# Optimization experiments

Measured on AMD Instinct MI355X. Metric: run time of the kernel, lower is better.

## Reference

```python
import jax, jax.numpy as jnp
import numpy as np
from functools import partial

S, E, K = 50000, 20000, 128
B = 16384
NE = 1000000
L = 2  # num_layer


def setup_inputs() -> dict:
    key = jax.random.key(0)
    ks = jax.random.split(key, 24)
    inp = {
        'stu_id': jax.random.randint(ks[0], (B,), 0, S),
        'input_exercise': jax.random.randint(ks[1], (B,), 0, E),
        'input_knowledge_point': jax.random.uniform(ks[2], (B, K), jnp.float32),
        'rows_1': jax.random.randint(ks[3], (NE,), 0, S),
        'cols_1': jax.random.randint(ks[4], (NE,), 0, E),
        'rows_0': jax.random.randint(ks[5], (NE,), 0, S),
        'cols_0': jax.random.randint(ks[6], (NE,), 0, E),
        'vals_ui_1': jax.random.uniform(ks[7], (NE,), jnp.float32),
        'vals_iu_1': jax.random.uniform(ks[8], (NE,), jnp.float32),
        'vals_ui_0': jax.random.uniform(ks[9], (NE,), jnp.float32),
        'vals_iu_0': jax.random.uniform(ks[10], (NE,), jnp.float32),
        'd_i_1': jax.random.uniform(ks[11], (S,), jnp.float32),
        'd_j_1': jax.random.uniform(ks[12], (E,), jnp.float32),
        'd_i_0': jax.random.uniform(ks[13], (S,), jnp.float32),
        'd_j_0': jax.random.uniform(ks[14], (E,), jnp.float32),
        'student_emb': jax.random.normal(ks[15], (S, K), jnp.float32) * 0.1,
        'exercise_emb': jax.random.normal(ks[16], (E, K), jnp.float32) * 0.1,
        'student_emb_bias': jax.random.normal(ks[17], (S, 1), jnp.float32) * 0.1,
        'e_discrimination': jax.random.normal(ks[18], (E, 1), jnp.float32) * 0.1,
        'W1': jax.random.normal(ks[19], (256, K), jnp.float32) * (1.0 / np.sqrt(K)),
        'b1': jnp.zeros((256,), jnp.float32),
        'W2': jax.random.normal(ks[20], (128, 256), jnp.float32) * (1.0 / np.sqrt(256)),
        'b2': jnp.zeros((128,), jnp.float32),
        'W3': jax.random.normal(ks[21], (1, 128), jnp.float32) * (1.0 / np.sqrt(128)),
        'b3': jnp.zeros((1,), jnp.float32),
    }
    return inp


def pos_linear(x, W, b):
    # PosLinear: weight = 2*relu(-W) + W  (== |W|)
    Wp = 2.0 * jax.nn.relu(-W) + W
    return x @ Wp.T + b


def spmm(vals, rows, cols, x, n_out):
    # sparse.mm(A, x) where A has entries vals at (rows, cols); gather cols of x, scatter-add to rows
    return jax.ops.segment_sum(vals[:, None] * x[cols], rows, num_segments=n_out)


def graph_repr(student_emb, exercise_emb,
               rows_1, cols_1, vals_ui_1, vals_iu_1,
               rows_0, cols_0, vals_ui_0, vals_iu_0,
               d_i_1, d_j_1, d_i_0, d_j_0):
    stat = student_emb          # [S, K]
    kdiff = exercise_emb        # [E, K]
    for _ in range(L):
        u1 = spmm(vals_ui_1, rows_1, cols_1, kdiff, S) + stat * d_i_1[:, None]
        i1 = spmm(vals_iu_1, cols_1, rows_1, stat, E) + kdiff * d_j_1[:, None]
        u0 = spmm(vals_ui_0, rows_0, cols_0, kdiff, S) + stat * d_i_0[:, None]
        i0 = spmm(vals_iu_0, cols_0, rows_0, stat, E) + kdiff * d_j_0[:, None]
        stat = u1 + u0
        kdiff = i1 + i0
    return stat, kdiff


def reference(stu_id, input_exercise, input_knowledge_point,
              rows_1, cols_1, rows_0, cols_0,
              vals_ui_1, vals_iu_1, vals_ui_0, vals_iu_0,
              d_i_1, d_j_1, d_i_0, d_j_0,
              student_emb, exercise_emb, student_emb_bias, e_discrimination,
              W1, b1, W2, b2, W3, b3):
    stat, kdiff = graph_repr(student_emb, exercise_emb,
                             rows_1, cols_1, vals_ui_1, vals_iu_1,
                             rows_0, cols_0, vals_ui_0, vals_iu_0,
                             d_i_1, d_j_1, d_i_0, d_j_0)
    e_disc = jax.nn.sigmoid(e_discrimination[input_exercise])          # [B, 1]
    stat_b = jax.nn.sigmoid(stat[stu_id] + student_emb_bias[stu_id])   # [B, K]
    kd = jax.nn.sigmoid(kdiff[input_exercise])                         # [B, K]
    x = input_knowledge_point * (stat_b - kd) * e_disc
    x = jnp.tanh(pos_linear(x, W1, b1))   # dropout is identity in eval
    x = jnp.tanh(pos_linear(x, W2, b2))
    out = jax.nn.sigmoid(pos_linear(x, W3, b3))
    return out.reshape(-1)
```

## Files before the change

### kernel.cpp

```cpp
#include <hip/hip_runtime.h>
#include <hip/hip_fp16.h>

#define S_N 50000
#define E_N 20000
#define K_N 128
#define B_N 16384
#define NE_N 1000000

#define S_PER_XCD 6250
#define E_PER_XCD 2500

#define SCAP 96
#define ECAP 176

#define NBKT 512
#define S_SUB 196
#define E_SUB 79
#define BKCAP 8704
#define OVL_BKTS 257

typedef short bf16x8 __attribute__((ext_vector_type(8)));
typedef float f32x4 __attribute__((ext_vector_type(4)));
typedef int i32x4 __attribute__((ext_vector_type(4)));
typedef float f32x4v __attribute__((ext_vector_type(4)));

__device__ __forceinline__ float sigmoidf_(float v) {
    return 1.0f / (1.0f + __expf(-v));
}
__device__ __forceinline__ float tanh_fast(float v) {
    float e = __expf(2.0f * v);
    return 1.0f - 2.0f / (e + 1.0f);
}
__device__ __forceinline__ unsigned short f2bf(float v) {
    unsigned u = __float_as_uint(v);
    u += 0x7fffu + ((u >> 16) & 1u);
    return (unsigned short)(u >> 16);
}
__device__ __forceinline__ void split_bf(float v, unsigned short& hi, unsigned short& lo) {
    unsigned u = __float_as_uint(v);
    hi = (unsigned short)(u >> 16);
    float fh = __uint_as_float(u & 0xffff0000u);
    lo = f2bf(v - fh);
}
__device__ __forceinline__ void accum8(float* acc, uint4 h, float v) {
    float2 p0 = __half22float2(*(const __half2*)&h.x);
    float2 p1 = __half22float2(*(const __half2*)&h.y);
    float2 p2 = __half22float2(*(const __half2*)&h.z);
    float2 p3 = __half22float2(*(const __half2*)&h.w);
    acc[0] = fmaf(v, p0.x, acc[0]); acc[1] = fmaf(v, p0.y, acc[1]);
    acc[2] = fmaf(v, p1.x, acc[2]); acc[3] = fmaf(v, p1.y, acc[3]);
    acc[4] = fmaf(v, p2.x, acc[4]); acc[5] = fmaf(v, p2.y, acc[5]);
    acc[6] = fmaf(v, p3.x, acc[6]); acc[7] = fmaf(v, p3.y, acc[7]);
}

__device__ __forceinline__ unsigned long long* bslot(
    unsigned long long* ovl, unsigned long long* fr, int b) {
    return (b < OVL_BKTS) ? ovl + (size_t)b * BKCAP
                          : fr + (size_t)(b - OVL_BKTS) * BKCAP;
}

__global__ __launch_bounds__(1024) void bucketize2(
    const i32x4* __restrict__ r1, const i32x4* __restrict__ c1,
    const f32x4v* __restrict__ vui1, const f32x4v* __restrict__ viu1,
    const i32x4* __restrict__ r0, const i32x4* __restrict__ c0,
    const f32x4v* __restrict__ vui0, const f32x4v* __restrict__ viu0,
    unsigned long long* __restrict__ bOvl, unsigned long long* __restrict__ bFr,
    int* __restrict__ gcur) {
    __shared__ int hist[NBKT];
    __shared__ int base[NBKT];
    const int tid = threadIdx.x;
    for (int b = tid; b < NBKT; b += 1024) hist[b] = 0;
    __syncthreads();
    const int NV = NE_N / 4;
    i32x4 rv[2], cv[2]; f32x4v av[2], bv[2];
    int bkt[16], lr[16];
#pragma unroll
    for (int rep = 0; rep < 2; ++rep) {
        int i = blockIdx.x * 2048 + rep * 1024 + tid;
        bool valid = i < 2 * NV;
        if (valid) {
            if (i < NV) {
                rv[rep] = __builtin_nontemporal_load(r1 + i);
                cv[rep] = __builtin_nontemporal_load(c1 + i);
                av[rep] = __builtin_nontemporal_load(vui1 + i);
                bv[rep] = __builtin_nontemporal_load(viu1 + i);
            } else {
                int j = i - NV;
                rv[rep] = __builtin_nontemporal_load(r0 + j);
                cv[rep] = __builtin_nontemporal_load(c0 + j);
                av[rep] = __builtin_nontemporal_load(vui0 + j);
                bv[rep] = __builtin_nontemporal_load(viu0 + j);
            }
        }
#pragma unroll
        for (int k = 0; k < 4; ++k) {
            int u = rep * 8 + k * 2;
            if (valid) {
                int r = rv[rep][k], c = cv[rep][k];
                int xs = r / S_PER_XCD;
                int ss = (r - xs * S_PER_XCD) / S_SUB;
                int xe = c / E_PER_XCD;
                int se = (c - xe * E_PER_XCD) / E_SUB;
                bkt[u] = ss * 8 + xs;
                bkt[u + 1] = 256 + se * 8 + xe;
                lr[u] = atomicAdd(&hist[bkt[u]], 1);
                lr[u + 1] = atomicAdd(&hist[bkt[u + 1]], 1);
            } else {
                bkt[u] = -1; bkt[u + 1] = -1;
            }
        }
    }
    __syncthreads();
    for (int b = tid; b < NBKT; b += 1024) {
        int h = hist[b];
        base[b] = h ? atomicAdd(&gcur[b], h) : 0;
    }
    __syncthreads();
#pragma unroll
    for (int rep = 0; rep < 2; ++rep) {
#pragma unroll
        for (int k = 0; k < 4; ++k) {
            int u = rep * 8 + k * 2;
            if (bkt[u] >= 0) {
                int r = rv[rep][k], c = cv[rep][k];
                unsigned entS = ((unsigned)f2bf(av[rep][k]) << 16) | (unsigned)c;
                unsigned entE = ((unsigned)f2bf(bv[rep][k]) << 16) | (unsigned)r;
                int pS = base[bkt[u]] + lr[u];
                int pE = base[bkt[u + 1]] + lr[u + 1];
                if (pS < BKCAP)
                    bslot(bOvl, bFr, bkt[u])[pS] =
                        ((unsigned long long)(unsigned)r << 32) | entS;
                if (pE < BKCAP)
                    bslot(bOvl, bFr, bkt[u + 1])[pE] =
                        ((unsigned long long)(unsigned)c << 32) | entE;
            }
        }
    }
}

__global__ __launch_bounds__(256) void scatter2(
    unsigned long long* __restrict__ bOvl, unsigned long long* __restrict__ bFr,
    const int* __restrict__ gcur,
    int* __restrict__ cntS, int* __restrict__ cntE,
    unsigned* __restrict__ csrS, unsigned* __restrict__ csrE) {
    __shared__ int lcnt[S_SUB];
    const int bid = blockIdx.x;
    const int tid = threadIdx.x;
    const bool isS = bid < 256;
    const int x = bid & 7;
    const int s = (isS ? bid : bid - 256) >> 3;
    const int start = isS ? x * S_PER_XCD + s * S_SUB : x * E_PER_XCD + s * E_SUB;
    const int len = isS ? min(S_SUB, S_PER_XCD - s * S_SUB)
                        : min(E_SUB, E_PER_XCD - s * E_SUB);
    for (int l = tid; l < len; l += 256) lcnt[l] = 0;
    __syncthreads();
    int n = gcur[bid];
    if (n > BKCAP) n = BKCAP;
    const unsigned long long* bp = bslot(bOvl, bFr, bid);
    for (int i = tid; i < n; i += 256) {
        unsigned long long v = __builtin_nontemporal_load(bp + i);
        int node = (int)(v >> 32);
        unsigned entry = (unsigned)v;
        int slot = atomicAdd(&lcnt[node - start], 1);
        if (isS) {
            if (slot < SCAP) csrS[(size_t)node * SCAP + slot] = entry;
        } else {
            if (slot < ECAP) csrE[(size_t)node * ECAP + slot] = entry;
        }
    }
    __syncthreads();
    for (int l = tid; l < len; l += 256) {
        if (isS) cntS[start + l] = lcnt[l];
        else     cntE[start + l] = lcnt[l];
    }
}

__global__ __launch_bounds__(256) void mark_needed2(
    const int* __restrict__ sid, const int* __restrict__ eid,
    unsigned* __restrict__ maskS, unsigned* __restrict__ maskE) {
    int i = blockIdx.x * blockDim.x + threadIdx.x;
    if (i < B_N) {
        int v = sid[i];
        atomicOr(&maskS[v >> 5], 1u << (v & 31));
    } else if (i < 2 * B_N) {
        int v = eid[i - B_N];
        atomicOr(&maskE[v >> 5], 1u << (v & 31));
    }
}

__global__ __launch_bounds__(256) void cvt_f16_init(
    const float2* __restrict__ sE, const float2* __restrict__ eE,
    __half2* __restrict__ sH, __half2* __restrict__ eH,
    int* __restrict__ cntS, int* __restrict__ cntE,
    unsigned* __restrict__ maskS, unsigned* __restrict__ maskE,
    int* __restrict__ cur) {
    int i = blockIdx.x * 256 + threadIdx.x;
    if (i < S_N) cntS[i] = 0;
    if (i < E_N) cntE[i] = 0;
    if (i < 2048) maskS[i] = 0;
    if (i < 1024) maskE[i] = 0;
    if (i < NBKT) cur[i] = 0;
    const int nS = S_N * 64;
    if (i < nS) {
        float2 v = sE[i];
        sH[i] = __floats2half2_rn(v.x, v.y);
    } else {
        int j = i - nS;
        if (j < E_N * 64) {
            float2 v = eE[j];
            eH[j] = __floats2half2_rn(v.x, v.y);
        }
    }
}

template<int CAP>
__global__ __launch_bounds__(256) void gather_pass_h4(
    const uint4* __restrict__ src, const uint4* __restrict__ self,
    const float* __restrict__ dA, const float* __restrict__ dB,
    const int* __restrict__ cnt, const unsigned* __restrict__ csr,
    const unsigned* __restrict__ need,
    uint4* __restrict__ dst, int nrow) {
    int w = blockIdx.x * 4 + (threadIdx.x >> 6);
    int lane = threadIdx.x & 63;
    int slot = lane >> 4;
    int seg = lane & 15;
    if (w >= nrow) return;
    if (need && !((need[w >> 5] >> (w & 31)) & 1u)) return;
    int n = cnt[w];
    if (n > CAP) n = CAP;
    const unsigned* cbase = csr + (size_t)w * CAP;
    float acc[8] = {};
    int i = 0;
    for (; i + 16 <= n; i += 16) {
        unsigned qa = __builtin_nontemporal_load(cbase + i + slot);
        unsigned qb = __builtin_nontemporal_load(cbase + i + 4 + slot);
        unsigned qc = __builtin_nontemporal_load(cbase + i + 8 + slot);
        unsigned qd = __builtin_nontemporal_load(cbase + i + 12 + slot);
        uint4 ha = src[(size_t)(qa & 0xffffu) * 16 + seg];
        uint4 hb = src[(size_t)(qb & 0xffffu) * 16 + seg];
        uint4 hc = src[(size_t)(qc & 0xffffu) * 16 + seg];
        uint4 hd = src[(size_t)(qd & 0xffffu) * 16 + seg];
        accum8(acc, ha, __uint_as_float(qa & 0xffff0000u));
        accum8(acc, hb, __uint_as_float(qb & 0xffff0000u));
        accum8(acc, hc, __uint_as_float(qc & 0xffff0000u));
        accum8(acc, hd, __uint_as_float(qd & 0xffff0000u));
    }
    for (; i + 8 <= n; i += 8) {
        unsigned qa = __builtin_nontemporal_load(cbase + i + slot);
        unsigned qb = __builtin_nontemporal_load(cbase + i + 4 + slot);
        uint4 ha = src[(size_t)(qa & 0xffffu) * 16 + seg];
        uint4 hb = src[(size_t)(qb & 0xffffu) * 16 + seg];
        accum8(acc, ha, __uint_as_float(qa & 0xffff0000u));
        accum8(acc, hb, __uint_as_float(qb & 0xffff0000u));
    }
    for (; i < n; i += 4) {
        int e = i + slot;
        if (e < n) {
            unsigned q = __builtin_nontemporal_load(cbase + e);
            uint4 h = src[(size_t)(q & 0xffffu) * 16 + seg];
            accum8(acc, h, __uint_as_float(q & 0xffff0000u));
        }
    }
#pragma unroll
    for (int j = 0; j < 8; ++j) {
        acc[j] += __shfl_xor(acc[j], 16);
        acc[j] += __shfl_xor(acc[j], 32);
    }
    if (slot == 0) {
        uint4 hs = self[(size_t)w * 16 + seg];
        float d = dA[w] + dB[w];
        float2 s0 = __half22float2(*(const __half2*)&hs.x);
        float2 s1 = __half22float2(*(const __half2*)&hs.y);
        float2 s2 = __half22float2(*(const __half2*)&hs.z);
        float2 s3 = __half22float2(*(const __half2*)&hs.w);
        uint4 o;
        *(__half2*)&o.x = __floats2half2_rn(fmaf(s0.x, d, acc[0]), fmaf(s0.y, d, acc[1]));
        *(__half2*)&o.y = __floats2half2_rn(fmaf(s1.x, d, acc[2]), fmaf(s1.y, d, acc[3]));
        *(__half2*)&o.z = __floats2half2_rn(fmaf(s2.x, d, acc[4]), fmaf(s2.y, d, acc[5]));
        *(__half2*)&o.w = __floats2half2_rn(fmaf(s3.x, d, acc[6]), fmaf(s3.y, d, acc[7]));
        dst[(size_t)w * 16 + seg] = o;
    }
}

__global__ __launch_bounds__(256) void abs_split_kernel(
    const float* __restrict__ W1, const float* __restrict__ W2,
    unsigned short* __restrict__ w1hi, unsigned short* __restrict__ w1lo,
    unsigned short* __restrict__ w2hi, unsigned short* __restrict__ w2lo) {
    int i = blockIdx.x * 256 + threadIdx.x;
    unsigned short hi, lo;
    if (i < 32768) {
        split_bf(fabsf(W1[i]), hi, lo);
        w1hi[i] = hi; w1lo[i] = lo;
    } else {
        int j = i - 32768;
        split_bf(fabsf(W2[j]), hi, lo);
        w2hi[j] = hi; w2lo[j] = lo;
    }
}

__global__ __launch_bounds__(256) void feature_kernel(
    const int* __restrict__ stu_id, const int* __restrict__ ex_id,
    const float* __restrict__ ikp,
    const __half2* __restrict__ statH, const __half2* __restrict__ kdiffH,
    const float* __restrict__ s_bias, const float* __restrict__ e_disc,
    unsigned short* __restrict__ xhi, unsigned short* __restrict__ xlo) {
    int i = blockIdx.x * 256 + threadIdx.x;
    int row = i >> 5;
    int k4 = (i & 31) * 4;
    int s = stu_id[row];
    int e = ex_id[row];
    float sb = s_bias[s];
    float ed = sigmoidf_(e_disc[e]);
    float2 s01 = __half22float2(statH[(size_t)s * 64 + (k4 >> 1)]);
    float2 s23 = __half22float2(statH[(size_t)s * 64 + (k4 >> 1) + 1]);
    float2 k01 = __half22float2(kdiffH[(size_t)e * 64 + (k4 >> 1)]);
    float2 k23 = __half22float2(kdiffH[(size_t)e * 64 + (k4 >> 1) + 1]);
    float4 iv = *(const float4*)(ikp + (size_t)row * K_N + k4);
    float f0 = iv.x * (sigmoidf_(s01.x + sb) - sigmoidf_(k01.x)) * ed;
    float f1 = iv.y * (sigmoidf_(s01.y + sb) - sigmoidf_(k01.y)) * ed;
    float f2 = iv.z * (sigmoidf_(s23.x + sb) - sigmoidf_(k23.x)) * ed;
    float f3 = iv.w * (sigmoidf_(s23.y + sb) - sigmoidf_(k23.y)) * ed;
    ushort4 oh, ol;
    split_bf(f0, oh.x, ol.x);
    split_bf(f1, oh.y, ol.y);
    split_bf(f2, oh.z, ol.z);
    split_bf(f3, oh.w, ol.w);
    *(ushort4*)(xhi + (size_t)row * K_N + k4) = oh;
    *(ushort4*)(xlo + (size_t)row * K_N + k4) = ol;
}

#define H1S 264

__global__ __launch_bounds__(256) void mlp_mfma(
    const unsigned short* __restrict__ xhi, const unsigned short* __restrict__ xlo,
    const unsigned short* __restrict__ w1hi, const unsigned short* __restrict__ w1lo,
    const unsigned short* __restrict__ w2hi, const unsigned short* __restrict__ w2lo,
    const float* __restrict__ b1, const float* __restrict__ b2,
    const float* __restrict__ W3, const float* __restrict__ b3,
    float* __restrict__ out) {
    __shared__ unsigned short h1hi[32 * H1S];
    __shared__ unsigned short h1lo[32 * H1S];
    __shared__ float partial[4][32];

    const int t = threadIdx.x;
    const int lane = t & 63;
    const int w = t >> 6;
    const int l15 = lane & 15;
    const int quad = lane >> 4;
    const int r0 = blockIdx.x * 32;

    f32x4 acc1[2][4] = {};
    for (int ks = 0; ks < 128; ks += 32) {
        bf16x8 ah[2], al[2], bh[4], bl[4];
#pragma unroll
        for (int mt = 0; mt < 2; ++mt) {
            size_t o = (size_t)(r0 + mt * 16 + l15) * K_N + ks + quad * 8;
            ah[mt] = *(const bf16x8*)(xhi + o);
            al[mt] = *(const bf16x8*)(xlo + o);
        }
#pragma unroll
        for (int nt = 0; nt < 4; ++nt) {
            size_t o = (size_t)(w * 64 + nt * 16 + l15) * 128 + ks + quad * 8;
            bh[nt] = *(const bf16x8*)(w1hi + o);
            bl[nt] = *(const bf16x8*)(w1lo + o);
        }
#pragma unroll
        for (int mt = 0; mt < 2; ++mt)
#pragma unroll
            for (int nt = 0; nt < 4; ++nt) {
                acc1[mt][nt] = __builtin_amdgcn_mfma_f32_16x16x32_bf16(
                    ah[mt], bh[nt], acc1[mt][nt], 0, 0, 0);
                acc1[mt][nt] = __builtin_amdgcn_mfma_f32_16x16x32_bf16(
                    ah[mt], bl[nt], acc1[mt][nt], 0, 0, 0);
                acc1[mt][nt] = __builtin_amdgcn_mfma_f32_16x16x32_bf16(
                    al[mt], bh[nt], acc1[mt][nt], 0, 0, 0);
            }
    }
#pragma unroll
    for (int nt = 0; nt < 4; ++nt) {
        int c = w * 64 + nt * 16 + l15;
        float bias = b1[c];
#pragma unroll
        for (int mt = 0; mt < 2; ++mt)
#pragma unroll
            for (int rg = 0; rg < 4; ++rg) {
                int row = mt * 16 + quad * 4 + rg;
                float h = tanh_fast(acc1[mt][nt][rg] + bias);
                unsigned short hi, lo;
                split_bf(h, hi, lo);
                h1hi[row * H1S + c] = hi;
                h1lo[row * H1S + c] = lo;
            }
    }
    __syncthreads();

    f32x4 acc2[2][2] = {};
    for (int ks = 0; ks < 256; ks += 32) {
        bf16x8 ah[2], al[2], bh[2], bl[2];
#pragma unroll
        for (int mt = 0; mt < 2; ++mt) {
            int o = (mt * 16 + l15) * H1S + ks + quad * 8;
            ah[mt] = *(const bf16x8*)(&h1hi[o]);
            al[mt] = *(const bf16x8*)(&h1lo[o]);
        }
#pragma unroll
        for (int nt = 0; nt < 2; ++nt) {
            size_t o = (size_t)(w * 32 + nt * 16 + l15) * 256 + ks + quad * 8;
            bh[nt] = *(const bf16x8*)(w2hi + o);
            bl[nt] = *(const bf16x8*)(w2lo + o);
        }
#pragma unroll
        for (int mt = 0; mt < 2; ++mt)
#pragma unroll
            for (int nt = 0; nt < 2; ++nt) {
                acc2[mt][nt] = __builtin_amdgcn_mfma_f32_16x16x32_bf16(
                    ah[mt], bh[nt], acc2[mt][nt], 0, 0, 0);
                acc2[mt][nt] = __builtin_amdgcn_mfma_f32_16x16x32_bf16(
                    ah[mt], bl[nt], acc2[mt][nt], 0, 0, 0);
                acc2[mt][nt] = __builtin_amdgcn_mfma_f32_16x16x32_bf16(
                    al[mt], bh[nt], acc2[mt][nt], 0, 0, 0);
            }
    }

    float w3v[2], b2v[2];
#pragma unroll
    for (int nt = 0; nt < 2; ++nt) {
        int c = w * 32 + nt * 16 + l15;
        w3v[nt] = fabsf(W3[c]);
        b2v[nt] = b2[c];
    }
#pragma unroll
    for (int mt = 0; mt < 2; ++mt)
#pragma unroll
        for (int rg = 0; rg < 4; ++rg) {
            float v = w3v[0] * tanh_fast(acc2[mt][0][rg] + b2v[0]) +
                      w3v[1] * tanh_fast(acc2[mt][1][rg] + b2v[1]);
            v += __shfl_xor(v, 1, 16);
            v += __shfl_xor(v, 2, 16);
            v += __shfl_xor(v, 4, 16);
            v += __shfl_xor(v, 8, 16);
            if (l15 == 0) partial[w][mt * 16 + quad * 4 + rg] = v;
        }
    __syncthreads();
    if (t < 32) {
        float v = partial[0][t] + partial[1][t] + partial[2][t] + partial[3][t];
        out[r0 + t] = sigmoidf_(v + b3[0]);
    }
}

extern "C" void kernel_launch(void* const* d_in, const int* in_sizes, int n_in,
                              void* d_out, int out_size, void* d_ws, size_t ws_size,
                              hipStream_t stream) {
    const int* stu_id        = (const int*)d_in[0];
    const int* input_ex      = (const int*)d_in[1];
    const float* ikp         = (const float*)d_in[2];
    const int* rows_1        = (const int*)d_in[3];
    const int* cols_1        = (const int*)d_in[4];
    const int* rows_0        = (const int*)d_in[5];
    const int* cols_0        = (const int*)d_in[6];
    const float* vals_ui_1   = (const float*)d_in[7];
    const float* vals_iu_1   = (const float*)d_in[8];
    const float* vals_ui_0   = (const float*)d_in[9];
    const float* vals_iu_0   = (const float*)d_in[10];
    const float* d_i_1       = (const float*)d_in[11];
    const float* d_j_1       = (const float*)d_in[12];
    const float* d_i_0       = (const float*)d_in[13];
    const float* d_j_0       = (const float*)d_in[14];
    const float* student_emb = (const float*)d_in[15];
    const float* exercise_emb= (const float*)d_in[16];
    const float* s_bias      = (const float*)d_in[17];
    const float* e_disc      = (const float*)d_in[18];
    const float* W1          = (const float*)d_in[19];
    const float* b1          = (const float*)d_in[20];
    const float* W2          = (const float*)d_in[21];
    const float* b2          = (const float*)d_in[22];
    const float* W3          = (const float*)d_in[23];
    const float* b3          = (const float*)d_in[24];

    char* p = (char*)d_ws;
    __half2* sEH     = (__half2*)p; p += (size_t)S_N * K_N * 2;
    __half2* eEH     = (__half2*)p; p += (size_t)E_N * K_N * 2;
    __half2* statAH  = (__half2*)p; p += (size_t)S_N * K_N * 2;
    __half2* kdiffAH = (__half2*)p; p += (size_t)E_N * K_N * 2;
    unsigned* csrS = (unsigned*)p; p += (size_t)S_N * SCAP * 4;
    unsigned* csrE = (unsigned*)p; p += (size_t)E_N * ECAP * 4;
    int* cntS     = (int*)p;   p += (size_t)S_N * 4;
    int* cntE     = (int*)p;   p += (size_t)E_N * 4;
    unsigned* maskS = (unsigned*)p; p += 2048 * 4;
    unsigned* maskE = (unsigned*)p; p += 1024 * 4;
    int* cur      = (int*)p;   p += NBKT * 4;
    p = (char*)(((size_t)p + 255) & ~(size_t)255);
    unsigned long long* buckFr = (unsigned long long*)p;
    p += (size_t)(NBKT - OVL_BKTS) * BKCAP * 8;
    unsigned long long* buckOvl = (unsigned long long*)statAH;
    __half2* statBH  = sEH;
    __half2* kdiffBH = eEH;
    unsigned short* xhi = (unsigned short*)statAH;
    unsigned short* xlo = xhi + (size_t)B_N * K_N;
    unsigned short* w1hi = (unsigned short*)kdiffAH;
    unsigned short* w1lo = w1hi + 32768;
    unsigned short* w2hi = w1lo + 32768;
    unsigned short* w2lo = w2hi + 32768;

    cvt_f16_init<<<((S_N + E_N) * 64 + 255) / 256, 256, 0, stream>>>(
        (const float2*)student_emb, (const float2*)exercise_emb, sEH, eEH,
        cntS, cntE, maskS, maskE, cur);

    const int bkBlocks = (2 * NE_N / 4 + 2047) / 2048;
    bucketize2<<<bkBlocks, 1024, 0, stream>>>(
        (const i32x4*)rows_1, (const i32x4*)cols_1,
        (const f32x4v*)vals_ui_1, (const f32x4v*)vals_iu_1,
        (const i32x4*)rows_0, (const i32x4*)cols_0,
        (const f32x4v*)vals_ui_0, (const f32x4v*)vals_iu_0,
        buckOvl, buckFr, cur);

    scatter2<<<NBKT, 256, 0, stream>>>(
        buckOvl, buckFr, cur, cntS, cntE, csrS, csrE);

    mark_needed2<<<(2 * B_N + 255) / 256, 256, 0, stream>>>(
        stu_id, input_ex, maskS, maskE);

    const int sGrid = (S_N + 3) / 4;
    const int eGrid = (E_N + 3) / 4;

    gather_pass_h4<SCAP><<<sGrid, 256, 0, stream>>>(
        (const uint4*)eEH, (const uint4*)sEH, d_i_1, d_i_0,
        cntS, csrS, nullptr, (uint4*)statAH, S_N);
    gather_pass_h4<ECAP><<<eGrid, 256, 0, stream>>>(
        (const uint4*)sEH, (const uint4*)eEH, d_j_1, d_j_0,
        cntE, csrE, nullptr, (uint4*)kdiffAH, E_N);

    gather_pass_h4<SCAP><<<sGrid, 256, 0, stream>>>(
        (const uint4*)kdiffAH, (const uint4*)statAH, d_i_1, d_i_0,
        cntS, csrS, maskS, (uint4*)statBH, S_N);
    gather_pass_h4<ECAP><<<eGrid, 256, 0, stream>>>(
        (const uint4*)statAH, (const uint4*)kdiffAH, d_j_1, d_j_0,
        cntE, csrE, maskE, (uint4*)kdiffBH, E_N);

    feature_kernel<<<B_N * 32 / 256, 256, 0, stream>>>(
        stu_id, input_ex, ikp, statBH, kdiffBH, s_bias, e_disc, xhi, xlo);
    abs_split_kernel<<<256, 256, 0, stream>>>(W1, W2, w1hi, w1lo, w2hi, w2lo);
    mlp_mfma<<<B_N / 32, 256, 0, stream>>>(xhi, xlo, w1hi, w1lo, w2hi, w2lo,
                                           b1, b2, W3, b3, (float*)d_out);
}
```

Measured before the change: 402.8 us.

## Split gather passes into source-range slices for cache locality

The adjacency lists are partitioned by source-node range: two slices for students and four for exercises. Each gather pass becomes several launches, one per slice, so the source embedding rows read by any one launch fit better in L2/MALL cache. Per-slice counts are packed into a single int, and later slices accumulate into the destination in fp16 with nontemporal stores. The cost is more kernel launches, repeated fp16 rounding across slices, and a read-modify-write of the output rows for every slice after the first.

```diff
diff --git a/kernel.cpp b/kernel.cpp
--- a/kernel.cpp
+++ b/kernel.cpp
@@ -10,8 +10,14 @@
 #define S_PER_XCD 6250
 #define E_PER_XCD 2500
 
-#define SCAP 96
-#define ECAP 176
+#define S_NSL 2
+#define SCAP_SL 44
+#define S_STRIDE 88
+#define E_HALF 10000
+#define E_NSL 4
+#define ECAP_SL 52
+#define E_STRIDE 208
+#define S_QUART 12500
 
 #define NBKT 512
 #define S_SUB 196
@@ -23,6 +29,7 @@
 typedef float f32x4 __attribute__((ext_vector_type(4)));
 typedef int i32x4 __attribute__((ext_vector_type(4)));
 typedef float f32x4v __attribute__((ext_vector_type(4)));
+typedef unsigned u32x4 __attribute__((ext_vector_type(4)));
 
 __device__ __forceinline__ float sigmoidf_(float v) {
     return 1.0f / (1.0f + __expf(-v));
@@ -143,7 +150,7 @@
     const int* __restrict__ gcur,
     int* __restrict__ cntS, int* __restrict__ cntE,
     unsigned* __restrict__ csrS, unsigned* __restrict__ csrE) {
-    __shared__ int lcnt[S_SUB];
+    __shared__ int lcnt[S_SUB * S_NSL];
     const int bid = blockIdx.x;
     const int tid = threadIdx.x;
     const bool isS = bid < 256;
@@ -152,26 +159,42 @@
     const int start = isS ? x * S_PER_XCD + s * S_SUB : x * E_PER_XCD + s * E_SUB;
     const int len = isS ? min(S_SUB, S_PER_XCD - s * S_SUB)
                         : min(E_SUB, E_PER_XCD - s * E_SUB);
-    for (int l = tid; l < len; l += 256) lcnt[l] = 0;
+    const int nsl = isS ? S_NSL : E_NSL;
+    for (int l = tid; l < len * nsl; l += 256) lcnt[l] = 0;
     __syncthreads();
     int n = gcur[bid];
     if (n > BKCAP) n = BKCAP;
     const unsigned long long* bp = bslot(bOvl, bFr, bid);
     for (int i = tid; i < n; i += 256) {
         unsigned long long v = __builtin_nontemporal_load(bp + i);
-        int node = (int)(v >> 32);
+        int node = (int)((v >> 32) & 0x7fffffffu);
         unsigned entry = (unsigned)v;
-        int slot = atomicAdd(&lcnt[node - start], 1);
+        int src = (int)(entry & 0xffffu);
         if (isS) {
-            if (slot < SCAP) csrS[(size_t)node * SCAP + slot] = entry;
+            int sl = (src >= E_HALF) ? 1 : 0;
+            int slot = atomicAdd(&lcnt[(node - start) * S_NSL + sl], 1);
+            if (slot < SCAP_SL)
+                csrS[(size_t)node * S_STRIDE + sl * SCAP_SL + slot] = entry;
         } else {
-            if (slot < ECAP) csrE[(size_t)node * ECAP + slot] = entry;
+            int sl = src / S_QUART;
+            int slot = atomicAdd(&lcnt[(node - start) * E_NSL + sl], 1);
+            if (slot < ECAP_SL)
+                csrE[(size_t)node * E_STRIDE + sl * ECAP_SL + slot] = entry;
         }
     }
     __syncthreads();
     for (int l = tid; l < len; l += 256) {
-        if (isS) cntS[start + l] = lcnt[l];
-        else     cntE[start + l] = lcnt[l];
+        if (isS) {
+            int c0 = min(lcnt[l * S_NSL], SCAP_SL);
+            int c1 = min(lcnt[l * S_NSL + 1], SCAP_SL);
+            cntS[start + l] = c0 | (c1 << 16);
+        } else {
+            int c0 = min(lcnt[l * E_NSL], ECAP_SL);
+            int c1 = min(lcnt[l * E_NSL + 1], ECAP_SL);
+            int c2 = min(lcnt[l * E_NSL + 2], ECAP_SL);
+            int c3 = min(lcnt[l * E_NSL + 3], ECAP_SL);
+            cntE[start + l] = c0 | (c1 << 8) | (c2 << 16) | (c3 << 24);
+        }
     }
 }
 
@@ -213,22 +236,24 @@
     }
 }
 
-template<int CAP>
-__global__ __launch_bounds__(256) void gather_pass_h4(
+template<int NSL, int SC, int BITS, bool FIRST>
+__global__ __launch_bounds__(256) void gather_slice(
     const uint4* __restrict__ src, const uint4* __restrict__ self,
     const float* __restrict__ dA, const float* __restrict__ dB,
     const int* __restrict__ cnt, const unsigned* __restrict__ csr,
     const unsigned* __restrict__ need,
-    uint4* __restrict__ dst, int nrow) {
+    uint4* __restrict__ dst, int nrow, int slice) {
     int w = blockIdx.x * 4 + (threadIdx.x >> 6);
     int lane = threadIdx.x & 63;
     int slot = lane >> 4;
     int seg = lane & 15;
     if (w >= nrow) return;
     if (need && !((need[w >> 5] >> (w & 31)) & 1u)) return;
-    int n = cnt[w];
-    if (n > CAP) n = CAP;
-    const unsigned* cbase = csr + (size_t)w * CAP;
+    unsigned pc = (unsigned)cnt[w];
+    int n = (int)((pc >> (slice * BITS)) & ((1u << BITS) - 1u));
+    if (n > SC) n = SC;
+    if (!FIRST && n == 0) return;
+    const unsigned* cbase = csr + (size_t)w * (NSL * SC) + slice * SC;
     float acc[8] = {};
     int i = 0;
     for (; i + 16 <= n; i += 16) {
@@ -267,18 +292,35 @@
         acc[j] += __shfl_xor(acc[j], 32);
     }
     if (slot == 0) {
-        uint4 hs = self[(size_t)w * 16 + seg];
-        float d = dA[w] + dB[w];
-        float2 s0 = __half22float2(*(const __half2*)&hs.x);
-        float2 s1 = __half22float2(*(const __half2*)&hs.y);
-        float2 s2 = __half22float2(*(const __half2*)&hs.z);
-        float2 s3 = __half22float2(*(const __half2*)&hs.w);
-        uint4 o;
-        *(__half2*)&o.x = __floats2half2_rn(fmaf(s0.x, d, acc[0]), fmaf(s0.y, d, acc[1]));
-        *(__half2*)&o.y = __floats2half2_rn(fmaf(s1.x, d, acc[2]), fmaf(s1.y, d, acc[3]));
-        *(__half2*)&o.z = __floats2half2_rn(fmaf(s2.x, d, acc[4]), fmaf(s2.y, d, acc[5]));
-        *(__half2*)&o.w = __floats2half2_rn(fmaf(s3.x, d, acc[6]), fmaf(s3.y, d, acc[7]));
-        dst[(size_t)w * 16 + seg] = o;
+        u32x4 o;
+        if (FIRST) {
+            uint4 hs = self[(size_t)w * 16 + seg];
+            float d = dA[w] + dB[w];
+            float2 s0 = __half22float2(*(const __half2*)&hs.x);
+            float2 s1 = __half22float2(*(const __half2*)&hs.y);
+            float2 s2 = __half22float2(*(const __half2*)&hs.z);
+            float2 s3 = __half22float2(*(const __half2*)&hs.w);
+            __half2 t0 = __floats2half2_rn(fmaf(s0.x, d, acc[0]), fmaf(s0.y, d, acc[1]));
+            __half2 t1 = __floats2half2_rn(fmaf(s1.x, d, acc[2]), fmaf(s1.y, d, acc[3]));
+            __half2 t2 = __floats2half2_rn(fmaf(s2.x, d, acc[4]), fmaf(s2.y, d, acc[5]));
+            __half2 t3 = __floats2half2_rn(fmaf(s3.x, d, acc[6]), fmaf(s3.y, d, acc[7]));
+            o.x = *(unsigned*)&t0; o.y = *(unsigned*)&t1;
+            o.z = *(unsigned*)&t2; o.w = *(unsigned*)&t3;
+        } else {
+            uint4 hs = dst[(size_t)w * 16 + seg];
+            float2 s0 = __half22float2(*(const __half2*)&hs.x);
+            float2 s1 = __half22float2(*(const __half2*)&hs.y);
+            float2 s2 = __half22float2(*(const __half2*)&hs.z);
+            float2 s3 = __half22float2(*(const __half2*)&hs.w);
+            __half2 t0 = __floats2half2_rn(s0.x + acc[0], s0.y + acc[1]);
+            __half2 t1 = __floats2half2_rn(s1.x + acc[2], s1.y + acc[3]);
+            __half2 t2 = __floats2half2_rn(s2.x + acc[4], s2.y + acc[5]);
+            __half2 t3 = __floats2half2_rn(s3.x + acc[6], s3.y + acc[7]);
+            o.x = *(unsigned*)&t0; o.y = *(unsigned*)&t1;
+            o.z = *(unsigned*)&t2; o.w = *(unsigned*)&t3;
+        }
+        __builtin_nontemporal_store(
+            o, reinterpret_cast<u32x4*>(dst) + ((size_t)w * 16 + seg));
     }
 }
 
@@ -482,8 +524,8 @@
     __half2* eEH     = (__half2*)p; p += (size_t)E_N * K_N * 2;
     __half2* statAH  = (__half2*)p; p += (size_t)S_N * K_N * 2;
     __half2* kdiffAH = (__half2*)p; p += (size_t)E_N * K_N * 2;
-    unsigned* csrS = (unsigned*)p; p += (size_t)S_N * SCAP * 4;
-    unsigned* csrE = (unsigned*)p; p += (size_t)E_N * ECAP * 4;
+    unsigned* csrS = (unsigned*)p; p += (size_t)S_N * S_STRIDE * 4;
+    unsigned* csrE = (unsigned*)p; p += (size_t)E_N * E_STRIDE * 4;
     int* cntS     = (int*)p;   p += (size_t)S_N * 4;
     int* cntE     = (int*)p;   p += (size_t)E_N * 4;
     unsigned* maskS = (unsigned*)p; p += 2048 * 4;
@@ -523,19 +565,33 @@
     const int sGrid = (S_N + 3) / 4;
     const int eGrid = (E_N + 3) / 4;
 
-    gather_pass_h4<SCAP><<<sGrid, 256, 0, stream>>>(
+    gather_slice<S_NSL, SCAP_SL, 16, true><<<sGrid, 256, 0, stream>>>(
         (const uint4*)eEH, (const uint4*)sEH, d_i_1, d_i_0,
-        cntS, csrS, nullptr, (uint4*)statAH, S_N);
-    gather_pass_h4<ECAP><<<eGrid, 256, 0, stream>>>(
+        cntS, csrS, nullptr, (uint4*)statAH, S_N, 0);
+    gather_slice<S_NSL, SCAP_SL, 16, false><<<sGrid, 256, 0, stream>>>(
+        (const uint4*)eEH, nullptr, nullptr, nullptr,
+        cntS, csrS, nullptr, (uint4*)statAH, S_N, 1);
+    gather_slice<E_NSL, ECAP_SL, 8, true><<<eGrid, 256, 0, stream>>>(
         (const uint4*)sEH, (const uint4*)eEH, d_j_1, d_j_0,
-        cntE, csrE, nullptr, (uint4*)kdiffAH, E_N);
-
-    gather_pass_h4<SCAP><<<sGrid, 256, 0, stream>>>(
+        cntE, csrE, nullptr, (uint4*)kdiffAH, E_N, 0);
+    for (int sl = 1; sl < E_NSL; ++sl)
+        gather_slice<E_NSL, ECAP_SL, 8, false><<<eGrid, 256, 0, stream>>>(
+            (const uint4*)sEH, nullptr, nullptr, nullptr,
+            cntE, csrE, nullptr, (uint4*)kdiffAH, E_N, sl);
+
+    gather_slice<S_NSL, SCAP_SL, 16, true><<<sGrid, 256, 0, stream>>>(
         (const uint4*)kdiffAH, (const uint4*)statAH, d_i_1, d_i_0,
-        cntS, csrS, maskS, (uint4*)statBH, S_N);
-    gather_pass_h4<ECAP><<<eGrid, 256, 0, stream>>>(
+        cntS, csrS, maskS, (uint4*)statBH, S_N, 0);
+    gather_slice<S_NSL, SCAP_SL, 16, false><<<sGrid, 256, 0, stream>>>(
+        (const uint4*)kdiffAH, nullptr, nullptr, nullptr,
+        cntS, csrS, maskS, (uint4*)statBH, S_N, 1);
+    gather_slice<E_NSL, ECAP_SL, 8, true><<<eGrid, 256, 0, stream>>>(
         (const uint4*)statAH, (const uint4*)kdiffAH, d_j_1, d_j_0,
-        cntE, csrE, maskE, (uint4*)kdiffBH, E_N);
+        cntE, csrE, maskE, (uint4*)kdiffBH, E_N, 0);
+    for (int sl = 1; sl < E_NSL; ++sl)
+        gather_slice<E_NSL, ECAP_SL, 8, false><<<eGrid, 256, 0, stream>>>(
+            (const uint4*)statAH, nullptr, nullptr, nullptr,
+            cntE, csrE, maskE, (uint4*)kdiffBH, E_N, sl);
 
     feature_kernel<<<B_N * 32 / 256, 256, 0, stream>>>(
         stu_id, input_ex, ikp, statBH, kdiffBH, s_bias, e_disc, xhi, xlo);
```

Result: slower. 470.7 us (+16.8%).
